# Kernel optimization log

Measured on AMD Instinct MI355X. Metric: run time of the kernel, lower is better.

Reference implementation:

```python
import jax, jax.numpy as jnp
import numpy as np

N_EMBD = 768
N_HEAD = 12
B, T = 2, 2048


def setup_inputs() -> dict:
    key = jax.random.key(0)
    ks = jax.random.split(key, 8)
    C = N_EMBD
    s = 0.02
    return {
        "x": jax.random.normal(ks[0], (B, T, C), jnp.float32),
        "ln1_g": jnp.ones((C,), jnp.float32),
        "ln1_b": jnp.zeros((C,), jnp.float32),
        "w_attn": jax.random.normal(ks[1], (C, 3 * C), jnp.float32) * s,
        "b_attn": jnp.zeros((3 * C,), jnp.float32),
        "w_attn_proj": jax.random.normal(ks[2], (C, C), jnp.float32) * s,
        "b_attn_proj": jnp.zeros((C,), jnp.float32),
        "ln2_g": jnp.ones((C,), jnp.float32),
        "ln2_b": jnp.zeros((C,), jnp.float32),
        "w_fc": jax.random.normal(ks[3], (C, 4 * C), jnp.float32) * s,
        "b_fc": jnp.zeros((4 * C,), jnp.float32),
        "w_mlp_proj": jax.random.normal(ks[4], (4 * C, C), jnp.float32) * s,
        "b_mlp_proj": jnp.zeros((C,), jnp.float32),
    }


def _layernorm(x, g, b, eps=1e-5):
    mu = jnp.mean(x, axis=-1, keepdims=True)
    var = jnp.mean(jnp.square(x - mu), axis=-1, keepdims=True)
    return (x - mu) * jax.lax.rsqrt(var + eps) * g + b


def _new_gelu(x):
    c = np.sqrt(2.0 / np.pi).astype(np.float32)
    return 0.5 * x * (1.0 + jnp.tanh(c * (x + 0.044715 * x * x * x)))


def _block(x, ln1_g, ln1_b, w_attn, b_attn, w_attn_proj, b_attn_proj,
           ln2_g, ln2_b, w_fc, b_fc, w_mlp_proj, b_mlp_proj):
    Bx, Tx, C = x.shape
    hd = C // N_HEAD
    h = _layernorm(x, ln1_g, ln1_b)
    qkv = h @ w_attn + b_attn  # [B,T,3C]
    q, k, v = jnp.split(qkv, 3, axis=-1)
    # [B,H,T,hd]
    q = q.reshape(Bx, Tx, N_HEAD, hd).transpose(0, 2, 1, 3)
    k = k.reshape(Bx, Tx, N_HEAD, hd).transpose(0, 2, 1, 3)
    v = v.reshape(Bx, Tx, N_HEAD, hd).transpose(0, 2, 1, 3)
    att = jnp.einsum('bhqd,bhkd->bhqk', q, k) * (1.0 / np.sqrt(hd))
    causal = jnp.tril(jnp.ones((Tx, Tx), bool))
    att = jnp.where(causal[None, None], att, -jnp.inf)
    att = jax.nn.softmax(att, axis=-1)
    y = jnp.einsum('bhqk,bhkd->bhqd', att, v)
    y = y.transpose(0, 2, 1, 3).reshape(Bx, Tx, C)
    x = x + y @ w_attn_proj + b_attn_proj
    h2 = _layernorm(x, ln2_g, ln2_b)
    x = x + _new_gelu(h2 @ w_fc + b_fc) @ w_mlp_proj + b_mlp_proj
    return x


def reference(x, ln1_g, ln1_b, w_attn, b_attn, w_attn_proj, b_attn_proj,
              ln2_g, ln2_b, w_fc, b_fc, w_mlp_proj, b_mlp_proj):
    return _block(x, ln1_g, ln1_b, w_attn, b_attn, w_attn_proj, b_attn_proj,
                  ln2_g, ln2_b, w_fc, b_fc, w_mlp_proj, b_mlp_proj)
```

## Files before the change

kernel.cpp:

```cpp
#include <hip/hip_runtime.h>
#include <hip/hip_bf16.h>
#include <math.h>

#define N_EMBD 768
#define N_HEAD 12
#define BATCH  2
#define SEQ    2048
#define ROWS   (BATCH*SEQ)
#define C3     (3*N_EMBD)

typedef __bf16 bf16;
typedef __attribute__((ext_vector_type(8))) __bf16 bf16x8;
typedef __attribute__((ext_vector_type(4))) float f32x4;

__device__ __forceinline__ void async16(const bf16* g, bf16* l) {
    __builtin_amdgcn_global_load_lds(
        (const __attribute__((address_space(1))) uint32_t*)g,
        (__attribute__((address_space(3))) uint32_t*)l, 16, 0, 0);
}

__global__ __launch_bounds__(256) void k_transpose_all(
    const float* __restrict__ w0, bf16* __restrict__ o0,
    const float* __restrict__ w1, bf16* __restrict__ o1,
    const float* __restrict__ w2, bf16* __restrict__ o2,
    const float* __restrict__ w3, bf16* __restrict__ o3)
{
    __shared__ bf16 tile[32][33];
    int bid = blockIdx.x;
    const float* in; bf16* out; int K, N, local;
    if      (bid < 1728) { in = w0; out = o0; K = 768;  N = 2304; local = bid; }
    else if (bid < 2304) { in = w1; out = o1; K = 768;  N = 768;  local = bid - 1728; }
    else if (bid < 4608) { in = w2; out = o2; K = 768;  N = 3072; local = bid - 2304; }
    else                 { in = w3; out = o3; K = 3072; N = 768;  local = bid - 4608; }
    int nt = N / 32;
    int n0 = (local % nt) * 32, k0 = (local / nt) * 32;
    int tc = threadIdx.x & 31, tr = threadIdx.x >> 5;
    #pragma unroll
    for (int i = 0; i < 4; i++) {
        int r = tr + i * 8;
        tile[r][tc] = (bf16)in[(size_t)(k0 + r) * N + n0 + tc];
    }
    __syncthreads();
    #pragma unroll
    for (int i = 0; i < 4; i++) {
        int r = tr + i * 8;
        out[(size_t)(n0 + r) * K + k0 + tc] = tile[tc][r];
    }
}

__global__ __launch_bounds__(256) void k_vtrans(
    const bf16* __restrict__ qkv, bf16* __restrict__ vt)
{
    __shared__ bf16 tile[32][33];
    int tt = blockIdx.x;
    int bh = blockIdx.y;
    int dt = blockIdx.z;
    int b = bh / N_HEAD, h = bh % N_HEAD;
    int tc = threadIdx.x & 31, tr = threadIdx.x >> 5;
    #pragma unroll
    for (int i = 0; i < 4; i++) {
        int r = tr + i * 8;
        tile[r][tc] = qkv[(size_t)(b * SEQ + tt * 32 + r) * C3 + 2 * N_EMBD + h * 64 + dt * 32 + tc];
    }
    __syncthreads();
    #pragma unroll
    for (int i = 0; i < 4; i++) {
        int r = tr + i * 8;
        vt[(size_t)(bh * 64 + dt * 32 + r) * SEQ + tt * 32 + tc] = tile[tc][r];
    }
}

__global__ __launch_bounds__(256) void k_layernorm(
    const float* __restrict__ x, const float* __restrict__ g,
    const float* __restrict__ b, bf16* __restrict__ out)
{
    int wave = threadIdx.x >> 6, lane = threadIdx.x & 63;
    int row = blockIdx.x * 4 + wave;
    const float* xr = x + (size_t)row * N_EMBD;
    float v[12];
    float s = 0.f, sq = 0.f;
    #pragma unroll
    for (int i = 0; i < 12; i++) {
        v[i] = xr[lane + 64 * i];
        s += v[i]; sq += v[i] * v[i];
    }
    #pragma unroll
    for (int off = 32; off > 0; off >>= 1) {
        s  += __shfl_xor(s, off);
        sq += __shfl_xor(sq, off);
    }
    float mu  = s * (1.f / N_EMBD);
    float var = sq * (1.f / N_EMBD) - mu * mu;
    float rs  = rsqrtf(var + 1e-5f);
    bf16* orow = out + (size_t)row * N_EMBD;
    #pragma unroll
    for (int i = 0; i < 12; i++) {
        int c = lane + 64 * i;
        orow[c] = (bf16)((v[i] - mu) * rs * g[c] + b[c]);
    }
}

template<int BN, int ACT, bool RES, bool OUT_BF16>
__global__ __launch_bounds__(256) void k_gemm(
    const bf16* __restrict__ A, const bf16* __restrict__ Bt,
    const float* __restrict__ bias, const float* __restrict__ res,
    void* __restrict__ outp, int M, int N, int K)
{
    constexpr int WC  = BN / 64;
    constexpr int WR  = 4 / WC;
    constexpr int RPW = 128 / WR;
    constexpr int MI  = RPW / 16;
    __shared__ __align__(16) bf16 As[128 * 64];
    __shared__ __align__(16) bf16 Bs[BN * 64];
    int n0 = blockIdx.x * BN, m0 = blockIdx.y * 128;
    int t = threadIdx.x;
    int lane = t & 63, wave = t >> 6;
    int wr = wave / WC, wc = wave % WC;
    int quad = lane >> 4, l16 = lane & 15;

    f32x4 acc[MI][4];
    #pragma unroll
    for (int i = 0; i < MI; i++)
        #pragma unroll
        for (int j = 0; j < 4; j++) acc[i][j] = (f32x4){0.f, 0.f, 0.f, 0.f};

    int sr = t >> 3;
    int sc = t & 7;
    int gsw = (sc ^ (sr & 7)) * 8;

    for (int k0 = 0; k0 < K; k0 += 64) {
        __syncthreads();
        #pragma unroll
        for (int p = 0; p < 4; p++) {
            int r = sr + p * 32;
            async16(&A[(size_t)(m0 + r) * K + k0 + gsw], &As[r * 64 + sc * 8]);
        }
        #pragma unroll
        for (int p = 0; p < BN / 32; p++) {
            int r = sr + p * 32;
            async16(&Bt[(size_t)(n0 + r) * K + k0 + gsw], &Bs[r * 64 + sc * 8]);
        }
        __syncthreads();
        #pragma unroll
        for (int kh = 0; kh < 2; kh++) {
            bf16x8 af[MI], bfv[4];
            #pragma unroll
            for (int i = 0; i < MI; i++)
                af[i]  = *(bf16x8*)&As[(wr * RPW + i * 16 + l16) * 64 + (((quad + 4 * kh) ^ (l16 & 7)) * 8)];
            #pragma unroll
            for (int j = 0; j < 4; j++)
                bfv[j] = *(bf16x8*)&Bs[(wc * 64 + j * 16 + l16) * 64 + (((quad + 4 * kh) ^ (l16 & 7)) * 8)];
            #pragma unroll
            for (int i = 0; i < MI; i++)
                #pragma unroll
                for (int j = 0; j < 4; j++)
                    acc[i][j] = __builtin_amdgcn_mfma_f32_16x16x32_bf16(af[i], bfv[j], acc[i][j], 0, 0, 0);
        }
    }

    float* outf = (float*)outp;
    bf16*  outb = (bf16*)outp;
    #pragma unroll
    for (int i = 0; i < MI; i++) {
        #pragma unroll
        for (int j = 0; j < 4; j++) {
            int col = n0 + wc * 64 + j * 16 + l16;
            float bv = bias[col];
            #pragma unroll
            for (int r = 0; r < 4; r++) {
                int row = m0 + wr * RPW + i * 16 + quad * 4 + r;
                float v = acc[i][j][r] + bv;
                if (ACT == 1) {
                    float z = 0.7978845608f * (v + 0.044715f * v * v * v);
                    v = v / (1.f + __expf(-2.f * z));
                }
                if (RES) v += res[(size_t)row * N + col];
                if (OUT_BF16) outb[(size_t)row * N + col] = (bf16)v;
                else          outf[(size_t)row * N + col] = v;
            }
        }
    }
}

#define PS_S 72
__global__ __launch_bounds__(256) void k_flash(
    const bf16* __restrict__ qkv, const bf16* __restrict__ vt, bf16* __restrict__ y)
{
    __shared__ __align__(16) bf16 Ks[2][64 * 64];
    __shared__ __align__(16) bf16 VTl[2][64 * 64];
    __shared__ __align__(16) bf16 Ps[4][16 * PS_S];
    int bid = blockIdx.x;
    int hi = bid >> 8;
    int lo = bid & 255;
    int g  = lo >> 3;
    int e  = lo & 7;
    int bh = hi * 8 + e;
    int qt;
    if      (hi == 0) qt = g;
    else if (hi == 1) qt = (g + 16) & 31;
    else              qt = (g < 16) ? (30 - 2 * g) : (63 - 2 * g);
    int b = bh / N_HEAD, h = bh % N_HEAD;
    int t = threadIdx.x, lane = t & 63, wave = t >> 6;
    int quad = lane >> 4, l16 = lane & 15;
    int qbase = qt * 64 + wave * 16;

    bf16x8 qa[2];
    {
        const bf16* qrow = qkv + (size_t)(b * SEQ + qbase + l16) * C3 + h * 64;
        #pragma unroll
        for (int kh = 0; kh < 2; kh++) {
            union { uint4 u4; bf16 e[8]; bf16x8 vv; } uq;
            uq.u4 = *(const uint4*)&qrow[quad * 8 + kh * 32];
            #pragma unroll
            for (int j = 0; j < 8; j++) uq.e[j] = (bf16)((float)uq.e[j] * 0.125f);
            qa[kh] = uq.vv;
        }
    }
    float l_part[4] = {0.f, 0.f, 0.f, 0.f};
    f32x4 o[4];
    #pragma unroll
    for (int j = 0; j < 4; j++) o[j] = (f32x4){0.f, 0.f, 0.f, 0.f};

    int sr = t >> 3;
    int sc = t & 7;
    int gsw = (sc ^ (sr & 7)) * 8;

    const bf16* kg = qkv + (size_t)b * SEQ * C3 + N_EMBD + h * 64;
    const bf16* vg = vt + (size_t)bh * 64 * SEQ;

    auto stage = [&](int tile, int bufi) {
        int k0 = tile * 64;
        #pragma unroll
        for (int p = 0; p < 2; p++) {
            int rr = sr + 32 * p;
            async16(&kg[(size_t)(k0 + rr) * C3 + gsw],  &Ks[bufi][rr * 64 + sc * 8]);
            async16(&vg[(size_t)rr * SEQ + k0 + gsw], &VTl[bufi][rr * 64 + sc * 8]);
        }
    };

    int ntiles = qt + 1;
    stage(0, 0);

    for (int tt = 0; tt < ntiles; tt++) {
        int bufi = tt & 1;
        int k0 = tt * 64;
        __syncthreads();
        if (tt + 1 < ntiles) stage(tt + 1, bufi ^ 1);

        f32x4 s[4];
        #pragma unroll
        for (int nt = 0; nt < 4; nt++) {
            bf16x8 b0 = *(bf16x8*)&Ks[bufi][(nt * 16 + l16) * 64 + (((quad    ) ^ (l16 & 7)) * 8)];
            bf16x8 b1 = *(bf16x8*)&Ks[bufi][(nt * 16 + l16) * 64 + (((quad + 4) ^ (l16 & 7)) * 8)];
            f32x4 z = (f32x4){0.f, 0.f, 0.f, 0.f};
            z = __builtin_amdgcn_mfma_f32_16x16x32_bf16(qa[0], b0, z, 0, 0, 0);
            z = __builtin_amdgcn_mfma_f32_16x16x32_bf16(qa[1], b1, z, 0, 0, 0);
            s[nt] = z;
        }
        bool diag = (tt == qt);
        float p[4][4];
        #pragma unroll
        for (int nt = 0; nt < 4; nt++) {
            int key = k0 + nt * 16 + l16;
            #pragma unroll
            for (int r = 0; r < 4; r++) {
                float pv = __expf(s[nt][r]);
                if (diag && key > qbase + quad * 4 + r) pv = 0.f;
                p[nt][r] = pv;
                l_part[r] += pv;
            }
        }
        #pragma unroll
        for (int nt = 0; nt < 4; nt++)
            #pragma unroll
            for (int r = 0; r < 4; r++)
                Ps[wave][(quad * 4 + r) * PS_S + nt * 16 + l16] = (bf16)p[nt][r];
        bf16x8 pa[2];
        #pragma unroll
        for (int kt = 0; kt < 2; kt++)
            pa[kt] = *(bf16x8*)&Ps[wave][l16 * PS_S + kt * 32 + quad * 8];
        #pragma unroll
        for (int jt = 0; jt < 4; jt++) {
            int d = jt * 16 + l16;
            #pragma unroll
            for (int kt = 0; kt < 2; kt++) {
                bf16x8 vb = *(bf16x8*)&VTl[bufi][d * 64 + (((quad + 4 * kt) ^ (l16 & 7)) * 8)];
                o[jt] = __builtin_amdgcn_mfma_f32_16x16x32_bf16(pa[kt], vb, o[jt], 0, 0, 0);
            }
        }
    }
    #pragma unroll
    for (int r = 0; r < 4; r++) {
        #pragma unroll
        for (int off = 8; off > 0; off >>= 1) l_part[r] += __shfl_xor(l_part[r], off);
    }
    #pragma unroll
    for (int jt = 0; jt < 4; jt++)
        #pragma unroll
        for (int r = 0; r < 4; r++) {
            int q = qbase + quad * 4 + r;
            y[(size_t)(b * SEQ + q) * N_EMBD + h * 64 + jt * 16 + l16] =
                (bf16)(o[jt][r] / l_part[r]);
        }
}

extern "C" void kernel_launch(void* const* d_in, const int* in_sizes, int n_in,
                              void* d_out, int out_size, void* d_ws, size_t ws_size,
                              hipStream_t stream) {
    const float* x           = (const float*)d_in[0];
    const float* ln1_g       = (const float*)d_in[1];
    const float* ln1_b       = (const float*)d_in[2];
    const float* w_attn      = (const float*)d_in[3];
    const float* b_attn      = (const float*)d_in[4];
    const float* w_attn_proj = (const float*)d_in[5];
    const float* b_attn_proj = (const float*)d_in[6];
    const float* ln2_g       = (const float*)d_in[7];
    const float* ln2_b       = (const float*)d_in[8];
    const float* w_fc        = (const float*)d_in[9];
    const float* b_fc        = (const float*)d_in[10];
    const float* w_mlp_proj  = (const float*)d_in[11];
    const float* b_mlp_proj  = (const float*)d_in[12];

    char* ws = (char*)d_ws;
    size_t off = 0;
    auto alloc = [&](size_t n) -> void* {
        off = (off + 255) & ~(size_t)255;
        void* p = ws + off;
        off += n;
        return p;
    };
    bf16* wqkvT  = (bf16*)alloc((size_t)C3 * N_EMBD * 2);
    bf16* wprojT = (bf16*)alloc((size_t)N_EMBD * N_EMBD * 2);
    bf16* wfcT   = (bf16*)alloc((size_t)4 * N_EMBD * N_EMBD * 2);
    bf16* wmlpT  = (bf16*)alloc((size_t)N_EMBD * 4 * N_EMBD * 2);
    bf16* hbuf   = (bf16*)alloc((size_t)ROWS * N_EMBD * 2);
    float* x2    = (float*)alloc((size_t)ROWS * N_EMBD * 4);
    bf16* yb     = (bf16*)alloc((size_t)ROWS * N_EMBD * 2);
    bf16* vtb    = (bf16*)alloc((size_t)BATCH * N_HEAD * 64 * SEQ * 2);
    bf16* big    = (bf16*)alloc((size_t)ROWS * 4 * N_EMBD * 2);
    bf16* qkvb   = big;
    bf16* actb   = big;

    k_transpose_all<<<6912, 256, 0, stream>>>(w_attn, wqkvT, w_attn_proj, wprojT,
                                              w_fc, wfcT, w_mlp_proj, wmlpT);

    k_layernorm<<<ROWS / 4, 256, 0, stream>>>(x, ln1_g, ln1_b, hbuf);
    k_gemm<128, 0, false, true ><<<dim3(C3 / 128,  ROWS / 128), 256, 0, stream>>>(
        hbuf, wqkvT,  b_attn,      nullptr, qkvb, ROWS, C3,     N_EMBD);
    k_vtrans<<<dim3(SEQ / 32, BATCH * N_HEAD, 2), 256, 0, stream>>>(qkvb, vtb);
    k_flash<<<768, 256, 0, stream>>>(qkvb, vtb, yb);
    k_gemm<64,  0, true,  false><<<dim3(N_EMBD / 64, ROWS / 128), 256, 0, stream>>>(
        yb,   wprojT, b_attn_proj, x,       x2,   ROWS, N_EMBD, N_EMBD);
    k_layernorm<<<ROWS / 4, 256, 0, stream>>>(x2, ln2_g, ln2_b, hbuf);
    k_gemm<128, 1, false, true ><<<dim3(3072 / 128, ROWS / 128), 256, 0, stream>>>(
        hbuf, wfcT,   b_fc,        nullptr, actb, ROWS, 3072,   N_EMBD);
    k_gemm<64,  0, true,  false><<<dim3(N_EMBD / 64, ROWS / 128), 256, 0, stream>>>(
        actb, wmlpT,  b_mlp_proj,  x2, (float*)d_out, ROWS, N_EMBD, 3072);
}
```

Before: 288.7 us.

## Split-K projection GEMMs with atomics and halve flash query tile size

The two N=768 projection GEMMs now use split-K of 2 over a third grid dimension. Partial sums are accumulated with float atomicAdd into outputs that are zeroed by memsets beforehand, and bias and residual are added only by the first split. The flash attention kernel moves to 32-query blocks with 2 waves (1536 blocks) and a new causal-balancing block order, but it drops the double-buffered K/V staging for a single buffer with an extra barrier. The aim is more blocks to fill the CUs, at the cost of atomic traffic, extra memsets and less load/compute overlap in attention.

```diff
diff --git a/kernel.cpp b/kernel.cpp
--- a/kernel.cpp
+++ b/kernel.cpp
@@ -100,7 +100,7 @@
     }
 }
 
-template<int BN, int ACT, bool RES, bool OUT_BF16>
+template<int BN, int ACT, bool RES, bool OUT_BF16, int SPLITK>
 __global__ __launch_bounds__(256) void k_gemm(
     const bf16* __restrict__ A, const bf16* __restrict__ Bt,
     const float* __restrict__ bias, const float* __restrict__ res,
@@ -128,7 +128,9 @@
     int sc = t & 7;
     int gsw = (sc ^ (sr & 7)) * 8;
 
-    for (int k0 = 0; k0 < K; k0 += 64) {
+    int kchunk = K / SPLITK;
+    int kbeg = blockIdx.z * kchunk;
+    for (int k0 = kbeg; k0 < kbeg + kchunk; k0 += 64) {
         __syncthreads();
         #pragma unroll
         for (int p = 0; p < 4; p++) {
@@ -169,50 +171,58 @@
             #pragma unroll
             for (int r = 0; r < 4; r++) {
                 int row = m0 + wr * RPW + i * 16 + quad * 4 + r;
-                float v = acc[i][j][r] + bv;
-                if (ACT == 1) {
-                    float z = 0.7978845608f * (v + 0.044715f * v * v * v);
-                    v = v / (1.f + __expf(-2.f * z));
+                float v = acc[i][j][r];
+                if (SPLITK > 1) {
+                    if (blockIdx.z == 0) {
+                        v += bv;
+                        if (RES) v += res[(size_t)row * N + col];
+                    }
+                    atomicAdd(&outf[(size_t)row * N + col], v);
+                } else {
+                    v += bv;
+                    if (ACT == 1) {
+                        float z = 0.7978845608f * (v + 0.044715f * v * v * v);
+                        v = v / (1.f + __expf(-2.f * z));
+                    }
+                    if (RES) v += res[(size_t)row * N + col];
+                    if (OUT_BF16) outb[(size_t)row * N + col] = (bf16)v;
+                    else          outf[(size_t)row * N + col] = v;
                 }
-                if (RES) v += res[(size_t)row * N + col];
-                if (OUT_BF16) outb[(size_t)row * N + col] = (bf16)v;
-                else          outf[(size_t)row * N + col] = v;
             }
         }
     }
 }
 
 #define PS_S 72
-__global__ __launch_bounds__(256) void k_flash(
+__global__ __launch_bounds__(128) void k_flash(
     const bf16* __restrict__ qkv, const bf16* __restrict__ vt, bf16* __restrict__ y)
 {
-    __shared__ __align__(16) bf16 Ks[2][64 * 64];
-    __shared__ __align__(16) bf16 VTl[2][64 * 64];
-    __shared__ __align__(16) bf16 Ps[4][16 * PS_S];
+    __shared__ __align__(16) bf16 Ks[64 * 64];
+    __shared__ __align__(16) bf16 VTl[64 * 64];
+    __shared__ __align__(16) bf16 Ps[2][16 * PS_S];
     int bid = blockIdx.x;
     int hi = bid >> 8;
     int lo = bid & 255;
-    int g  = lo >> 3;
-    int e  = lo & 7;
-    int bh = hi * 8 + e;
-    int qt;
-    if      (hi == 0) qt = g;
-    else if (hi == 1) qt = (g + 16) & 31;
-    else              qt = (g < 16) ? (30 - 2 * g) : (63 - 2 * g);
+    int g  = lo >> 2;
+    int e  = lo & 3;
+    int bh = hi * 4 + e;
+    int rot = (hi >> 1) * 21;
+    int gs = (g + rot) & 63;
+    int qt = (hi & 1) ? 63 - gs : gs;
     int b = bh / N_HEAD, h = bh % N_HEAD;
     int t = threadIdx.x, lane = t & 63, wave = t >> 6;
     int quad = lane >> 4, l16 = lane & 15;
-    int qbase = qt * 64 + wave * 16;
+    int qbase = qt * 32 + wave * 16;
 
     bf16x8 qa[2];
     {
         const bf16* qrow = qkv + (size_t)(b * SEQ + qbase + l16) * C3 + h * 64;
         #pragma unroll
         for (int kh = 0; kh < 2; kh++) {
-            union { uint4 u4; bf16 e[8]; bf16x8 vv; } uq;
+            union { uint4 u4; bf16 e8[8]; bf16x8 vv; } uq;
             uq.u4 = *(const uint4*)&qrow[quad * 8 + kh * 32];
             #pragma unroll
-            for (int j = 0; j < 8; j++) uq.e[j] = (bf16)((float)uq.e[j] * 0.125f);
+            for (int j = 0; j < 8; j++) uq.e8[j] = (bf16)((float)uq.e8[j] * 0.125f);
             qa[kh] = uq.vv;
         }
     }
@@ -228,36 +238,29 @@
     const bf16* kg = qkv + (size_t)b * SEQ * C3 + N_EMBD + h * 64;
     const bf16* vg = vt + (size_t)bh * 64 * SEQ;
 
-    auto stage = [&](int tile, int bufi) {
-        int k0 = tile * 64;
-        #pragma unroll
-        for (int p = 0; p < 2; p++) {
-            int rr = sr + 32 * p;
-            async16(&kg[(size_t)(k0 + rr) * C3 + gsw],  &Ks[bufi][rr * 64 + sc * 8]);
-            async16(&vg[(size_t)rr * SEQ + k0 + gsw], &VTl[bufi][rr * 64 + sc * 8]);
-        }
-    };
-
-    int ntiles = qt + 1;
-    stage(0, 0);
-
+    int ntiles = (qt >> 1) + 1;
     for (int tt = 0; tt < ntiles; tt++) {
-        int bufi = tt & 1;
         int k0 = tt * 64;
         __syncthreads();
-        if (tt + 1 < ntiles) stage(tt + 1, bufi ^ 1);
+        #pragma unroll
+        for (int p = 0; p < 4; p++) {
+            int rr = sr + 16 * p;
+            async16(&kg[(size_t)(k0 + rr) * C3 + gsw],  &Ks[rr * 64 + sc * 8]);
+            async16(&vg[(size_t)rr * SEQ + k0 + gsw], &VTl[rr * 64 + sc * 8]);
+        }
+        __syncthreads();
 
         f32x4 s[4];
         #pragma unroll
         for (int nt = 0; nt < 4; nt++) {
-            bf16x8 b0 = *(bf16x8*)&Ks[bufi][(nt * 16 + l16) * 64 + (((quad    ) ^ (l16 & 7)) * 8)];
-            bf16x8 b1 = *(bf16x8*)&Ks[bufi][(nt * 16 + l16) * 64 + (((quad + 4) ^ (l16 & 7)) * 8)];
+            bf16x8 b0 = *(bf16x8*)&Ks[(nt * 16 + l16) * 64 + (((quad    ) ^ (l16 & 7)) * 8)];
+            bf16x8 b1 = *(bf16x8*)&Ks[(nt * 16 + l16) * 64 + (((quad + 4) ^ (l16 & 7)) * 8)];
             f32x4 z = (f32x4){0.f, 0.f, 0.f, 0.f};
             z = __builtin_amdgcn_mfma_f32_16x16x32_bf16(qa[0], b0, z, 0, 0, 0);
             z = __builtin_amdgcn_mfma_f32_16x16x32_bf16(qa[1], b1, z, 0, 0, 0);
             s[nt] = z;
         }
-        bool diag = (tt == qt);
+        bool diag = (tt == ntiles - 1);
         float p[4][4];
         #pragma unroll
         for (int nt = 0; nt < 4; nt++) {
@@ -284,7 +287,7 @@
             int d = jt * 16 + l16;
             #pragma unroll
             for (int kt = 0; kt < 2; kt++) {
-                bf16x8 vb = *(bf16x8*)&VTl[bufi][d * 64 + (((quad + 4 * kt) ^ (l16 & 7)) * 8)];
+                bf16x8 vb = *(bf16x8*)&VTl[d * 64 + (((quad + 4 * kt) ^ (l16 & 7)) * 8)];
                 o[jt] = __builtin_amdgcn_mfma_f32_16x16x32_bf16(pa[kt], vb, o[jt], 0, 0, 0);
             }
         }
@@ -344,16 +347,19 @@
     k_transpose_all<<<6912, 256, 0, stream>>>(w_attn, wqkvT, w_attn_proj, wprojT,
                                               w_fc, wfcT, w_mlp_proj, wmlpT);
 
+    hipMemsetAsync(x2,    0, (size_t)ROWS * N_EMBD * 4, stream);
+    hipMemsetAsync(d_out, 0, (size_t)ROWS * N_EMBD * 4, stream);
+
     k_layernorm<<<ROWS / 4, 256, 0, stream>>>(x, ln1_g, ln1_b, hbuf);
-    k_gemm<128, 0, false, true ><<<dim3(C3 / 128,  ROWS / 128), 256, 0, stream>>>(
+    k_gemm<128, 0, false, true,  1><<<dim3(C3 / 128,  ROWS / 128), 256, 0, stream>>>(
         hbuf, wqkvT,  b_attn,      nullptr, qkvb, ROWS, C3,     N_EMBD);
     k_vtrans<<<dim3(SEQ / 32, BATCH * N_HEAD, 2), 256, 0, stream>>>(qkvb, vtb);
-    k_flash<<<768, 256, 0, stream>>>(qkvb, vtb, yb);
-    k_gemm<64,  0, true,  false><<<dim3(N_EMBD / 64, ROWS / 128), 256, 0, stream>>>(
+    k_flash<<<1536, 128, 0, stream>>>(qkvb, vtb, yb);
+    k_gemm<64,  0, true,  false, 2><<<dim3(N_EMBD / 64, ROWS / 128, 2), 256, 0, stream>>>(
         yb,   wprojT, b_attn_proj, x,       x2,   ROWS, N_EMBD, N_EMBD);
     k_layernorm<<<ROWS / 4, 256, 0, stream>>>(x2, ln2_g, ln2_b, hbuf);
-    k_gemm<128, 1, false, true ><<<dim3(3072 / 128, ROWS / 128), 256, 0, stream>>>(
+    k_gemm<128, 1, false, true,  1><<<dim3(3072 / 128, ROWS / 128), 256, 0, stream>>>(
         hbuf, wfcT,   b_fc,        nullptr, actb, ROWS, 3072,   N_EMBD);
-    k_gemm<64,  0, true,  false><<<dim3(N_EMBD / 64, ROWS / 128), 256, 0, stream>>>(
+    k_gemm<64,  0, true,  false, 2><<<dim3(N_EMBD / 64, ROWS / 128, 2), 256, 0, stream>>>(
         actb, wmlpT,  b_mlp_proj,  x2, (float*)d_out, ROWS, N_EMBD, 3072);
 }
```

Measured after the change: 306.6 us. 6.2% more time.

## Halve GEMM K-tile to 32 with new swizzle and vectorize layernorm

Applied to the files above, without the earlier changes.

The GEMM K step drops from 64 to 32, which halves the LDS footprint per block and adjusts the XOR swizzle to a 4-chunk row layout. The aim is lower LDS use so more blocks fit per CU. The cost is twice as many barrier pairs per K and fewer MFMAs between syncs, with no double-buffering. The layernorm now loads and stores with float4 and packed bf16 vectors, which cuts memory instructions.

```diff
diff --git a/kernel.cpp b/kernel.cpp
--- a/kernel.cpp
+++ b/kernel.cpp
@@ -76,13 +76,16 @@
 {
     int wave = threadIdx.x >> 6, lane = threadIdx.x & 63;
     int row = blockIdx.x * 4 + wave;
-    const float* xr = x + (size_t)row * N_EMBD;
-    float v[12];
+    const float4* xr = (const float4*)(x + (size_t)row * N_EMBD);
+    const float4* g4 = (const float4*)g;
+    const float4* b4 = (const float4*)b;
+    float4 v[3];
     float s = 0.f, sq = 0.f;
     #pragma unroll
-    for (int i = 0; i < 12; i++) {
+    for (int i = 0; i < 3; i++) {
         v[i] = xr[lane + 64 * i];
-        s += v[i]; sq += v[i] * v[i];
+        s  += v[i].x + v[i].y + v[i].z + v[i].w;
+        sq += v[i].x * v[i].x + v[i].y * v[i].y + v[i].z * v[i].z + v[i].w * v[i].w;
     }
     #pragma unroll
     for (int off = 32; off > 0; off >>= 1) {
@@ -94,9 +97,14 @@
     float rs  = rsqrtf(var + 1e-5f);
     bf16* orow = out + (size_t)row * N_EMBD;
     #pragma unroll
-    for (int i = 0; i < 12; i++) {
-        int c = lane + 64 * i;
-        orow[c] = (bf16)((v[i] - mu) * rs * g[c] + b[c]);
+    for (int i = 0; i < 3; i++) {
+        float4 gv = g4[lane + 64 * i], bv = b4[lane + 64 * i];
+        union { ushort4 u4; bf16 e[4]; } pk;
+        pk.e[0] = (bf16)((v[i].x - mu) * rs * gv.x + bv.x);
+        pk.e[1] = (bf16)((v[i].y - mu) * rs * gv.y + bv.y);
+        pk.e[2] = (bf16)((v[i].z - mu) * rs * gv.z + bv.z);
+        pk.e[3] = (bf16)((v[i].w - mu) * rs * gv.w + bv.w);
+        *(ushort4*)&orow[(lane + 64 * i) * 4] = pk.u4;
     }
 }
 
@@ -110,8 +118,8 @@
     constexpr int WR  = 4 / WC;
     constexpr int RPW = 128 / WR;
     constexpr int MI  = RPW / 16;
-    __shared__ __align__(16) bf16 As[128 * 64];
-    __shared__ __align__(16) bf16 Bs[BN * 64];
+    __shared__ __align__(16) bf16 As[128 * 32];
+    __shared__ __align__(16) bf16 Bs[BN * 32];
     int n0 = blockIdx.x * BN, m0 = blockIdx.y * 128;
     int t = threadIdx.x;
     int lane = t & 63, wave = t >> 6;
@@ -124,38 +132,36 @@
         #pragma unroll
         for (int j = 0; j < 4; j++) acc[i][j] = (f32x4){0.f, 0.f, 0.f, 0.f};
 
-    int sr = t >> 3;
-    int sc = t & 7;
-    int gsw = (sc ^ (sr & 7)) * 8;
-
-    for (int k0 = 0; k0 < K; k0 += 64) {
+    int sr = t >> 2;
+    int sc = t & 3;
+    int gsw = ((sc ^ ((sr ^ (sr >> 2)) & 3))) * 8;
+    int rsw = (quad ^ ((l16 ^ (l16 >> 2)) & 3)) * 8;
+
+    for (int k0 = 0; k0 < K; k0 += 32) {
         __syncthreads();
         #pragma unroll
-        for (int p = 0; p < 4; p++) {
-            int r = sr + p * 32;
-            async16(&A[(size_t)(m0 + r) * K + k0 + gsw], &As[r * 64 + sc * 8]);
-        }
-        #pragma unroll
-        for (int p = 0; p < BN / 32; p++) {
-            int r = sr + p * 32;
-            async16(&Bt[(size_t)(n0 + r) * K + k0 + gsw], &Bs[r * 64 + sc * 8]);
+        for (int p = 0; p < 2; p++) {
+            int r = sr + p * 64;
+            async16(&A[(size_t)(m0 + r) * K + k0 + gsw], &As[r * 32 + sc * 8]);
+        }
+        #pragma unroll
+        for (int p = 0; p < BN / 64; p++) {
+            int r = sr + p * 64;
+            async16(&Bt[(size_t)(n0 + r) * K + k0 + gsw], &Bs[r * 32 + sc * 8]);
         }
         __syncthreads();
-        #pragma unroll
-        for (int kh = 0; kh < 2; kh++) {
-            bf16x8 af[MI], bfv[4];
-            #pragma unroll
-            for (int i = 0; i < MI; i++)
-                af[i]  = *(bf16x8*)&As[(wr * RPW + i * 16 + l16) * 64 + (((quad + 4 * kh) ^ (l16 & 7)) * 8)];
+        bf16x8 af[MI], bfv[4];
+        #pragma unroll
+        for (int i = 0; i < MI; i++)
+            af[i]  = *(bf16x8*)&As[(wr * RPW + i * 16 + l16) * 32 + rsw];
+        #pragma unroll
+        for (int j = 0; j < 4; j++)
+            bfv[j] = *(bf16x8*)&Bs[(wc * 64 + j * 16 + l16) * 32 + rsw];
+        #pragma unroll
+        for (int i = 0; i < MI; i++)
             #pragma unroll
             for (int j = 0; j < 4; j++)
-                bfv[j] = *(bf16x8*)&Bs[(wc * 64 + j * 16 + l16) * 64 + (((quad + 4 * kh) ^ (l16 & 7)) * 8)];
-            #pragma unroll
-            for (int i = 0; i < MI; i++)
-                #pragma unroll
-                for (int j = 0; j < 4; j++)
-                    acc[i][j] = __builtin_amdgcn_mfma_f32_16x16x32_bf16(af[i], bfv[j], acc[i][j], 0, 0, 0);
-        }
+                acc[i][j] = __builtin_amdgcn_mfma_f32_16x16x32_bf16(af[i], bfv[j], acc[i][j], 0, 0, 0);
     }
 
     float* outf = (float*)outp;
@@ -209,10 +215,10 @@
         const bf16* qrow = qkv + (size_t)(b * SEQ + qbase + l16) * C3 + h * 64;
         #pragma unroll
         for (int kh = 0; kh < 2; kh++) {
-            union { uint4 u4; bf16 e[8]; bf16x8 vv; } uq;
+            union { uint4 u4; bf16 e8[8]; bf16x8 vv; } uq;
             uq.u4 = *(const uint4*)&qrow[quad * 8 + kh * 32];
             #pragma unroll
-            for (int j = 0; j < 8; j++) uq.e[j] = (bf16)((float)uq.e[j] * 0.125f);
+            for (int j = 0; j < 8; j++) uq.e8[j] = (bf16)((float)uq.e8[j] * 0.125f);
             qa[kh] = uq.vv;
         }
     }
```

Result: slower. 308.3 us (+6.8%).
